# Kernel tuning notes

Measured on AMD Instinct MI355X. Metric: run time of the kernel, lower is better.

The kernel has to match this reference:

```python
import jax, jax.numpy as jnp
import numpy as np

B = 16          # graphs per batch
N = 8192        # nodes per graph (equal-size graphs)
D = 256         # in_channels
RATIO = 0.5
K = int(np.ceil(RATIO * N))   # nodes kept per graph (PyG: ceil(ratio*N))
E = 2_097_152   # total edges (~avg_degree 16)


def setup_inputs() -> dict:
    key = jax.random.key(0)
    k1, k2, k3 = jax.random.split(key, 3)
    x = jax.random.normal(k1, (B * N, D), dtype=jnp.float32)
    # edges confined within each graph: local endpoint ids + graph offset
    local = jax.random.randint(k2, (2, E), 0, N)
    graph_of_edge = jnp.arange(E) // (E // B)            # [E]
    edge_index = local + graph_of_edge[None, :] * N      # [2, E] global node ids
    batch = jnp.repeat(jnp.arange(B), N)                 # [B*N]
    weight = jax.random.normal(k3, (D,), dtype=jnp.float32)  # TopKPooling score weight
    return {"x": x, "edge_index": edge_index, "batch": batch, "weight": weight}


def reference(x, edge_index, batch, weight):
    total = x.shape[0]
    # PyG TopKPooling: score = tanh((x . w) / ||w||)
    score = jnp.tanh((x @ weight) / jnp.linalg.norm(weight))   # [B*N]
    # per-graph top-k (equal-size graphs -> reshape)
    vals, idx = jax.lax.top_k(score.reshape(B, N), K)          # [B, K] each
    perm = (idx + jnp.arange(B)[:, None] * N).reshape(-1)      # [B*K] global kept ids
    x_out = x[perm] * vals.reshape(-1, 1)                      # gate features by score
    batch_out = batch[perm]
    # reindex: kept node i (in perm order) gets new id i, others -1 (PyG filter_adj)
    mapping = jnp.full((total,), -1, dtype=jnp.int32).at[perm].set(
        jnp.arange(B * K, dtype=jnp.int32))
    new_src = mapping[edge_index[0]]
    new_dst = mapping[edge_index[1]]
    kept = (new_src >= 0) & (new_dst >= 0)
    # fixed-shape padded edge_index: surviving edges reindexed, dropped edges = -1
    new_edge_index = jnp.where(kept[None, :], jnp.stack([new_src, new_dst]), -1)
    return x_out, new_edge_index, batch_out
```

## Files before the change

### kernel.cpp

```cpp
#include <hip/hip_runtime.h>

#define BGRAPH  16
#define NPG     8192
#define DIM     256
#define KKEEP   4096
#define TOTALN  (BGRAPH * NPG)
#define TOTKEEP (BGRAPH * KKEEP)
#define NEDGE   2097152
#define NBUCK   8192

using u16 = unsigned short;
using u32 = unsigned int;

__device__ __forceinline__ u32 desc_key(float f) {
  u32 b = __float_as_uint(f);
  u32 s = b ^ ((b & 0x80000000u) ? 0xFFFFFFFFu : 0x80000000u);
  return ~s;
}

__global__ __launch_bounds__(256) void k_score(const float* __restrict__ x,
                                               const float* __restrict__ w,
                                               float* __restrict__ score) {
  int gid  = blockIdx.x * 256 + threadIdx.x;
  int row  = gid >> 6;
  int lane = gid & 63;
  const float4 x4 = *reinterpret_cast<const float4*>(x + (size_t)row * DIM + lane * 4);
  const float4 w4 = *reinterpret_cast<const float4*>(w + lane * 4);
  double dot = (double)x4.x * w4.x + (double)x4.y * w4.y
             + (double)x4.z * w4.z + (double)x4.w * w4.w;
  double w2  = (double)w4.x * w4.x + (double)w4.y * w4.y
             + (double)w4.z * w4.z + (double)w4.w * w4.w;
  #pragma unroll
  for (int off = 32; off > 0; off >>= 1) {
    dot += __shfl_xor(dot, off, 64);
    w2  += __shfl_xor(w2,  off, 64);
  }
  if (lane == 0) score[row] = tanhf((float)(dot / sqrt(w2)));
}

__global__ __launch_bounds__(1024) void k_sort(const float* __restrict__ score,
                                               u32* __restrict__ skey,
                                               u32* __restrict__ bends,
                                               u32* __restrict__ gceil) {
  __shared__ u32 hist[NBUCK];
  __shared__ u32 wsum[16];
  const int g    = blockIdx.x;
  const int tid  = threadIdx.x;
  const int wid  = tid >> 6;
  const int lane = tid & 63;
  const float* gs = score + ((size_t)g << 13);
  u32* skg = skey  + ((size_t)g << 13);
  u32* beg = bends + ((size_t)g << 13);

  #pragma unroll
  for (int i = 0; i < NBUCK / 1024; ++i) hist[tid + i * 1024] = 0;
  __syncthreads();

  u32 kd_[NPG / 1024];
  #pragma unroll
  for (int i = 0; i < NPG / 1024; ++i) {
    kd_[i] = desc_key(gs[tid + i * 1024]);
    atomicAdd(&hist[kd_[i] >> 19], 1u);
  }
  __syncthreads();

  u32 h[8], s = 0;
  #pragma unroll
  for (int j = 0; j < 8; ++j) { h[j] = hist[8 * tid + j]; s += h[j]; }
  u32 inc = s;
  #pragma unroll
  for (int off = 1; off < 64; off <<= 1) {
    u32 t = __shfl_up(inc, off, 64);
    if (lane >= off) inc += t;
  }
  if (lane == 63) wsum[wid] = inc;
  __syncthreads();
  if (tid < 16) {
    u32 v = wsum[tid], vi = v;
    #pragma unroll
    for (int off = 1; off < 16; off <<= 1) {
      u32 t = __shfl_up(vi, off, 64);
      if (tid >= off) vi += t;
    }
    wsum[tid] = vi - v;
  }
  __syncthreads();
  u32 run = inc - s + wsum[wid];
  #pragma unroll
  for (int j = 0; j < 8; ++j) {
    u32 hv  = h[j];
    u32 end = run + hv;
    hist[8 * tid + j] = run;
    beg[8 * tid + j]  = end;
    if (run < KKEEP && end >= KKEEP) gceil[g] = end;
    run = end;
  }
  __syncthreads();

  #pragma unroll
  for (int i = 0; i < NPG / 1024; ++i) {
    int idx = tid + i * 1024;
    u32 kd  = kd_[i];
    u32 pos = atomicAdd(&hist[kd >> 19], 1u);
    skg[pos] = (kd << 13) | (u32)idx;
  }
}

__global__ __launch_bounds__(512) void k_count(const float* __restrict__ score,
                                               const u32* __restrict__ skey,
                                               const u32* __restrict__ bends,
                                               const u32* __restrict__ gceil,
                                               u16* __restrict__ map16) {
  const int g = blockIdx.x >> 4;
  const int p = (blockIdx.x & 15) * 512 + (int)threadIdx.x;
  const size_t gb = ((size_t)g << 13);
  const u32* skg = skey + gb;
  u32 key = skg[p];
  int idx = (int)(key & 0x1FFFu);
  u16* mp = map16 + gb;
  if ((u32)p >= gceil[g]) { mp[idx] = (u16)0xFFFFu; return; }
  u32 b = desc_key(score[gb + idx]) >> 19;
  const u32* beg = bends + gb;
  u32 start = b ? beg[b - 1] : 0;
  u32 end   = beg[b];
  u32 cnt = 0, q = start;
  for (; q + 4 <= end; q += 4) {
    cnt += (skg[q]     < key) + (skg[q + 1] < key)
         + (skg[q + 2] < key) + (skg[q + 3] < key);
  }
  for (; q < end; ++q) cnt += (skg[q] < key);
  u32 rank = start + cnt;
  mp[idx] = (rank < KKEEP) ? (u16)rank : (u16)0xFFFFu;
}

__global__ __launch_bounds__(256) void k_gather(const float* __restrict__ x,
                                                const float* __restrict__ score,
                                                const u16* __restrict__ map16,
                                                float* __restrict__ x_out) {
  int gid  = blockIdx.x * 256 + threadIdx.x;
  int node = gid >> 6;
  int lane = gid & 63;
  u16 rk = map16[node];
  if (rk == 0xFFFFu) return;
  int nid = ((node >> 13) << 12) | (int)rk;
  float val = score[node];
  const float4 v = *reinterpret_cast<const float4*>(x + (size_t)node * DIM + lane * 4);
  float4 o;
  o.x = v.x * val; o.y = v.y * val; o.z = v.z * val; o.w = v.w * val;
  *reinterpret_cast<float4*>(x_out + (size_t)nid * DIM + lane * 4) = o;
}

__global__ __launch_bounds__(256) void k_edges(const int* __restrict__ ei,
                                               const u16* __restrict__ map16,
                                               float* __restrict__ e_out,
                                               float* __restrict__ b_out) {
  int t = blockIdx.x * 256 + threadIdx.x;
  const int4 a = *reinterpret_cast<const int4*>(ei + 4 * (size_t)t);
  const int4 b = *reinterpret_cast<const int4*>(ei + NEDGE + 4 * (size_t)t);
  u16 ra0 = map16[a.x], ra1 = map16[a.y], ra2 = map16[a.z], ra3 = map16[a.w];
  u16 rb0 = map16[b.x], rb1 = map16[b.y], rb2 = map16[b.z], rb3 = map16[b.w];
  float4 eo0, eo1;
  eo0.x = (ra0 != 0xFFFFu && rb0 != 0xFFFFu) ? (float)(((a.x >> 13) << 12) | ra0) : -1.0f;
  eo0.y = (ra1 != 0xFFFFu && rb1 != 0xFFFFu) ? (float)(((a.y >> 13) << 12) | ra1) : -1.0f;
  eo0.z = (ra2 != 0xFFFFu && rb2 != 0xFFFFu) ? (float)(((a.z >> 13) << 12) | ra2) : -1.0f;
  eo0.w = (ra3 != 0xFFFFu && rb3 != 0xFFFFu) ? (float)(((a.w >> 13) << 12) | ra3) : -1.0f;
  eo1.x = (ra0 != 0xFFFFu && rb0 != 0xFFFFu) ? (float)(((b.x >> 13) << 12) | rb0) : -1.0f;
  eo1.y = (ra1 != 0xFFFFu && rb1 != 0xFFFFu) ? (float)(((b.y >> 13) << 12) | rb1) : -1.0f;
  eo1.z = (ra2 != 0xFFFFu && rb2 != 0xFFFFu) ? (float)(((b.z >> 13) << 12) | rb2) : -1.0f;
  eo1.w = (ra3 != 0xFFFFu && rb3 != 0xFFFFu) ? (float)(((b.w >> 13) << 12) | rb3) : -1.0f;
  *reinterpret_cast<float4*>(e_out + 4 * (size_t)t)         = eo0;
  *reinterpret_cast<float4*>(e_out + NEDGE + 4 * (size_t)t) = eo1;
  if (t < TOTKEEP / 4) {
    float4 bo;
    bo.x = (float)((4 * t)     >> 12);
    bo.y = (float)((4 * t + 1) >> 12);
    bo.z = (float)((4 * t + 2) >> 12);
    bo.w = (float)((4 * t + 3) >> 12);
    *reinterpret_cast<float4*>(b_out + 4 * (size_t)t) = bo;
  }
}

extern "C" void kernel_launch(void* const* d_in, const int* in_sizes, int n_in,
                              void* d_out, int out_size, void* d_ws, size_t ws_size,
                              hipStream_t stream) {
  const float* x  = nullptr;
  const int*   ei = nullptr;
  const float* w  = nullptr;
  for (int i = 0; i < n_in; ++i) {
    if      (in_sizes[i] == TOTALN * DIM) x  = (const float*)d_in[i];
    else if (in_sizes[i] == 2 * NEDGE)    ei = (const int*)d_in[i];
    else if (in_sizes[i] == DIM)          w  = (const float*)d_in[i];
  }
  (void)out_size; (void)ws_size;

  float* out   = (float*)d_out;
  float* x_out = out;
  float* e_out = out + (size_t)TOTKEEP * DIM;
  float* b_out = e_out + 2 * (size_t)NEDGE;

  char* ws = (char*)d_ws;
  float* score = (float*)(ws);
  u32*   skey  = (u32*)(ws + (512  << 10));
  u32*   bends = (u32*)(ws + (1024 << 10));
  u16*   map16 = (u16*)(ws + (1536 << 10));
  u32*   gceil = (u32*)(ws + (1792 << 10));

  hipLaunchKernelGGL(k_score,  dim3(TOTALN / 4),  dim3(256),  0, stream, x, w, score);
  hipLaunchKernelGGL(k_sort,   dim3(BGRAPH),      dim3(1024), 0, stream, score, skey, bends, gceil);
  hipLaunchKernelGGL(k_count,  dim3(BGRAPH * 16), dim3(512),  0, stream, score, skey, bends, gceil, map16);
  hipLaunchKernelGGL(k_gather, dim3(TOTALN / 4),  dim3(256),  0, stream, x, score, map16, x_out);
  hipLaunchKernelGGL(k_edges,  dim3(NEDGE / 1024),dim3(256),  0, stream, ei, map16, e_out, b_out);
}
```

Before: 92.84 us.

## Split per-graph bucket sort across eight blocks per graph

```diff
diff --git a/kernel.cpp b/kernel.cpp
--- a/kernel.cpp
+++ b/kernel.cpp
@@ -8,6 +8,7 @@
 #define TOTKEEP (BGRAPH * KKEEP)
 #define NEDGE   2097152
 #define NBUCK   8192
+#define SCHUNK  8
 
 using u16 = unsigned short;
 using u32 = unsigned int;
@@ -43,8 +44,9 @@
                                                u32* __restrict__ bends,
                                                u32* __restrict__ gceil) {
   __shared__ u32 hist[NBUCK];
-  __shared__ u32 wsum[16];
-  const int g    = blockIdx.x;
+  __shared__ u32 acc[NBUCK];
+  const int g    = blockIdx.x >> 3;
+  const int c    = blockIdx.x & (SCHUNK - 1);
   const int tid  = threadIdx.x;
   const int wid  = tid >> 6;
   const int lane = tid & 63;
@@ -53,57 +55,68 @@
   u32* beg = bends + ((size_t)g << 13);
 
   #pragma unroll
-  for (int i = 0; i < NBUCK / 1024; ++i) hist[tid + i * 1024] = 0;
-  __syncthreads();
-
-  u32 kd_[NPG / 1024];
-  #pragma unroll
-  for (int i = 0; i < NPG / 1024; ++i) {
-    kd_[i] = desc_key(gs[tid + i * 1024]);
-    atomicAdd(&hist[kd_[i] >> 19], 1u);
+  for (int i = 0; i < NBUCK / 1024; ++i) {
+    hist[tid + i * 1024] = 0;
+    acc[tid + i * 1024]  = 0;
+  }
+  __syncthreads();
+
+  u32 mykd = 0;
+  #pragma unroll
+  for (int c2 = 0; c2 < SCHUNK; ++c2) {
+    u32 kd = desc_key(gs[c2 * 1024 + tid]);
+    atomicAdd(&hist[kd >> 19], 1u);
+    if (c2 == c) mykd = kd;
+    if (c2 < c)  atomicAdd(&acc[kd >> 19], 1u);
   }
   __syncthreads();
 
   u32 h[8], s = 0;
   #pragma unroll
   for (int j = 0; j < 8; ++j) { h[j] = hist[8 * tid + j]; s += h[j]; }
+  __syncthreads();
   u32 inc = s;
   #pragma unroll
   for (int off = 1; off < 64; off <<= 1) {
     u32 t = __shfl_up(inc, off, 64);
     if (lane >= off) inc += t;
   }
-  if (lane == 63) wsum[wid] = inc;
+  if (lane == 63) hist[wid] = inc;
   __syncthreads();
   if (tid < 16) {
-    u32 v = wsum[tid], vi = v;
+    u32 v = hist[tid], vi = v;
     #pragma unroll
     for (int off = 1; off < 16; off <<= 1) {
       u32 t = __shfl_up(vi, off, 64);
       if (tid >= off) vi += t;
     }
-    wsum[tid] = vi - v;
-  }
-  __syncthreads();
-  u32 run = inc - s + wsum[wid];
+    hist[tid] = vi - v;
+  }
+  __syncthreads();
+  u32 excl = inc - s + hist[wid];
+  __syncthreads();
+  u32 run = excl;
   #pragma unroll
   for (int j = 0; j < 8; ++j) {
-    u32 hv  = h[j];
-    u32 end = run + hv;
+    u32 end = run + h[j];
     hist[8 * tid + j] = run;
-    beg[8 * tid + j]  = end;
-    if (run < KKEEP && end >= KKEEP) gceil[g] = end;
+    if (c == 0) {
+      beg[8 * tid + j] = end;
+      if (run < KKEEP && end >= KKEEP) gceil[g] = end;
+    }
     run = end;
   }
   __syncthreads();
 
   #pragma unroll
-  for (int i = 0; i < NPG / 1024; ++i) {
-    int idx = tid + i * 1024;
-    u32 kd  = kd_[i];
-    u32 pos = atomicAdd(&hist[kd >> 19], 1u);
-    skg[pos] = (kd << 13) | (u32)idx;
-  }
+  for (int i = 0; i < NBUCK / 1024; ++i) {
+    int b = tid + i * 1024;
+    acc[b] += hist[b];
+  }
+  __syncthreads();
+
+  u32 pos = atomicAdd(&acc[mykd >> 19], 1u);
+  skg[pos] = (mykd << 13) | (u32)(c * 1024 + tid);
 }
 
 __global__ __launch_bounds__(512) void k_count(const float* __restrict__ score,
@@ -205,9 +218,9 @@
   u16*   map16 = (u16*)(ws + (1536 << 10));
   u32*   gceil = (u32*)(ws + (1792 << 10));
 
-  hipLaunchKernelGGL(k_score,  dim3(TOTALN / 4),  dim3(256),  0, stream, x, w, score);
-  hipLaunchKernelGGL(k_sort,   dim3(BGRAPH),      dim3(1024), 0, stream, score, skey, bends, gceil);
-  hipLaunchKernelGGL(k_count,  dim3(BGRAPH * 16), dim3(512),  0, stream, score, skey, bends, gceil, map16);
-  hipLaunchKernelGGL(k_gather, dim3(TOTALN / 4),  dim3(256),  0, stream, x, score, map16, x_out);
-  hipLaunchKernelGGL(k_edges,  dim3(NEDGE / 1024),dim3(256),  0, stream, ei, map16, e_out, b_out);
-}
+  hipLaunchKernelGGL(k_score,  dim3(TOTALN / 4),        dim3(256),  0, stream, x, w, score);
+  hipLaunchKernelGGL(k_sort,   dim3(BGRAPH * SCHUNK),   dim3(1024), 0, stream, score, skey, bends, gceil);
+  hipLaunchKernelGGL(k_count,  dim3(BGRAPH * 16),       dim3(512),  0, stream, score, skey, bends, gceil, map16);
+  hipLaunchKernelGGL(k_gather, dim3(TOTALN / 4),        dim3(256),  0, stream, x, score, map16, x_out);
+  hipLaunchKernelGGL(k_edges,  dim3(NEDGE / 1024),      dim3(256),  0, stream, ei, map16, e_out, b_out);
+}
```

Measured after the change: 91.12 us. Within noise of the previous version (-1.9%).

## Fuse all phases into one cooperative persistent kernel with grid syncs

Applied to the files above, without the earlier changes.

```diff
diff --git a/kernel.cpp b/kernel.cpp
--- a/kernel.cpp
+++ b/kernel.cpp
@@ -1,4 +1,7 @@
 #include <hip/hip_runtime.h>
+#include <hip/hip_cooperative_groups.h>
+
+namespace cg = cooperative_groups;
 
 #define BGRAPH  16
 #define NPG     8192
@@ -9,6 +12,9 @@
 #define NEDGE   2097152
 #define NBUCK   8192
 
+#define NBLK    256
+#define NTHR    1024
+
 using u16 = unsigned short;
 using u32 = unsigned int;
 
@@ -18,34 +24,37 @@
   return ~s;
 }
 
-__global__ __launch_bounds__(256) void k_score(const float* __restrict__ x,
-                                               const float* __restrict__ w,
-                                               float* __restrict__ score) {
-  int gid  = blockIdx.x * 256 + threadIdx.x;
-  int row  = gid >> 6;
-  int lane = gid & 63;
-  const float4 x4 = *reinterpret_cast<const float4*>(x + (size_t)row * DIM + lane * 4);
+__device__ __forceinline__ void phase_score(int gwave, int lane,
+                                            const float* __restrict__ x,
+                                            const float* __restrict__ w,
+                                            float* __restrict__ score) {
   const float4 w4 = *reinterpret_cast<const float4*>(w + lane * 4);
-  double dot = (double)x4.x * w4.x + (double)x4.y * w4.y
-             + (double)x4.z * w4.z + (double)x4.w * w4.w;
-  double w2  = (double)w4.x * w4.x + (double)w4.y * w4.y
-             + (double)w4.z * w4.z + (double)w4.w * w4.w;
-  #pragma unroll
-  for (int off = 32; off > 0; off >>= 1) {
-    dot += __shfl_xor(dot, off, 64);
-    w2  += __shfl_xor(w2,  off, 64);
-  }
-  if (lane == 0) score[row] = tanhf((float)(dot / sqrt(w2)));
-}
-
-__global__ __launch_bounds__(1024) void k_sort(const float* __restrict__ score,
-                                               u32* __restrict__ skey,
-                                               u32* __restrict__ bends,
-                                               u32* __restrict__ gceil) {
+  double w2 = (double)w4.x * w4.x + (double)w4.y * w4.y
+            + (double)w4.z * w4.z + (double)w4.w * w4.w;
+  #pragma unroll
+  for (int off = 32; off > 0; off >>= 1) w2 += __shfl_xor(w2, off, 64);
+  const double rn = sqrt(w2);
+  #pragma unroll 4
+  for (int i = 0; i < 32; ++i) {
+    int row = gwave * 32 + i;
+    const float4 x4 = *reinterpret_cast<const float4*>(x + (size_t)row * DIM + lane * 4);
+    double dot = (double)x4.x * w4.x + (double)x4.y * w4.y
+               + (double)x4.z * w4.z + (double)x4.w * w4.w;
+    #pragma unroll
+    for (int off = 32; off > 0; off >>= 1) dot += __shfl_xor(dot, off, 64);
+    if (lane == 0) score[row] = tanhf((float)(dot / rn));
+  }
+}
+
+__device__ __forceinline__ void phase_sort(int blk, int tid,
+                                           const float* __restrict__ score,
+                                           u32* __restrict__ skey,
+                                           u32* __restrict__ bends,
+                                           u32* __restrict__ gceil) {
   __shared__ u32 hist[NBUCK];
   __shared__ u32 wsum[16];
-  const int g    = blockIdx.x;
-  const int tid  = threadIdx.x;
+  if (blk >= BGRAPH) return;
+  const int g    = blk;
   const int wid  = tid >> 6;
   const int lane = tid & 63;
   const float* gs = score + ((size_t)g << 13);
@@ -53,13 +62,13 @@
   u32* beg = bends + ((size_t)g << 13);
 
   #pragma unroll
-  for (int i = 0; i < NBUCK / 1024; ++i) hist[tid + i * 1024] = 0;
-  __syncthreads();
-
-  u32 kd_[NPG / 1024];
-  #pragma unroll
-  for (int i = 0; i < NPG / 1024; ++i) {
-    kd_[i] = desc_key(gs[tid + i * 1024]);
+  for (int i = 0; i < NBUCK / NTHR; ++i) hist[tid + i * NTHR] = 0;
+  __syncthreads();
+
+  u32 kd_[NPG / NTHR];
+  #pragma unroll
+  for (int i = 0; i < NPG / NTHR; ++i) {
+    kd_[i] = desc_key(gs[tid + i * NTHR]);
     atomicAdd(&hist[kd_[i] >> 19], 1u);
   }
   __syncthreads();
@@ -98,27 +107,28 @@
   __syncthreads();
 
   #pragma unroll
-  for (int i = 0; i < NPG / 1024; ++i) {
-    int idx = tid + i * 1024;
-    u32 kd  = kd_[i];
-    u32 pos = atomicAdd(&hist[kd >> 19], 1u);
-    skg[pos] = (kd << 13) | (u32)idx;
-  }
-}
-
-__global__ __launch_bounds__(512) void k_count(const float* __restrict__ score,
-                                               const u32* __restrict__ skey,
-                                               const u32* __restrict__ bends,
-                                               const u32* __restrict__ gceil,
-                                               u16* __restrict__ map16) {
-  const int g = blockIdx.x >> 4;
-  const int p = (blockIdx.x & 15) * 512 + (int)threadIdx.x;
+  for (int i = 0; i < NPG / NTHR; ++i) {
+    int idx = tid + i * NTHR;
+    u32 pos = atomicAdd(&hist[kd_[i] >> 19], 1u);
+    skg[pos] = (kd_[i] << 13) | (u32)idx;
+  }
+}
+
+__device__ __forceinline__ void phase_count(int t,
+                                            const float* __restrict__ score,
+                                            const u32* __restrict__ skey,
+                                            const u32* __restrict__ bends,
+                                            const u32* __restrict__ gceil,
+                                            u16* __restrict__ map16,
+                                            u16* __restrict__ inv) {
+  if (t >= TOTALN) return;
+  const int g = t >> 13;
+  const int p = t & (NPG - 1);
   const size_t gb = ((size_t)g << 13);
   const u32* skg = skey + gb;
   u32 key = skg[p];
   int idx = (int)(key & 0x1FFFu);
-  u16* mp = map16 + gb;
-  if ((u32)p >= gceil[g]) { mp[idx] = (u16)0xFFFFu; return; }
+  if ((u32)p >= gceil[g]) { map16[gb + idx] = (u16)0xFFFFu; return; }
   u32 b = desc_key(score[gb + idx]) >> 19;
   const u32* beg = bends + gb;
   u32 start = b ? beg[b - 1] : 0;
@@ -130,54 +140,118 @@
   }
   for (; q < end; ++q) cnt += (skg[q] < key);
   u32 rank = start + cnt;
-  mp[idx] = (rank < KKEEP) ? (u16)rank : (u16)0xFFFFu;
-}
-
-__global__ __launch_bounds__(256) void k_gather(const float* __restrict__ x,
-                                                const float* __restrict__ score,
-                                                const u16* __restrict__ map16,
-                                                float* __restrict__ x_out) {
-  int gid  = blockIdx.x * 256 + threadIdx.x;
-  int node = gid >> 6;
-  int lane = gid & 63;
-  u16 rk = map16[node];
-  if (rk == 0xFFFFu) return;
-  int nid = ((node >> 13) << 12) | (int)rk;
-  float val = score[node];
-  const float4 v = *reinterpret_cast<const float4*>(x + (size_t)node * DIM + lane * 4);
-  float4 o;
-  o.x = v.x * val; o.y = v.y * val; o.z = v.z * val; o.w = v.w * val;
-  *reinterpret_cast<float4*>(x_out + (size_t)nid * DIM + lane * 4) = o;
-}
-
-__global__ __launch_bounds__(256) void k_edges(const int* __restrict__ ei,
-                                               const u16* __restrict__ map16,
+  if (rank < KKEEP) {
+    map16[gb + idx] = (u16)rank;
+    inv[((u32)g << 12) | rank] = (u16)idx;
+  } else {
+    map16[gb + idx] = (u16)0xFFFFu;
+  }
+}
+
+__device__ __forceinline__ void phase_gather(int gwave, int lane,
+                                             const float* __restrict__ x,
+                                             const float* __restrict__ score,
+                                             const u16* __restrict__ inv,
+                                             float* __restrict__ x_out) {
+  #pragma unroll 4
+  for (int i = 0; i < 16; ++i) {
+    int r = gwave * 16 + i;
+    int idx  = (int)inv[r];
+    int node = ((r >> 12) << 13) | idx;
+    float val = score[node];
+    const float4 v = *reinterpret_cast<const float4*>(x + (size_t)node * DIM + lane * 4);
+    float4 o;
+    o.x = v.x * val; o.y = v.y * val; o.z = v.z * val; o.w = v.w * val;
+    *reinterpret_cast<float4*>(x_out + (size_t)r * DIM + lane * 4) = o;
+  }
+}
+
+__device__ __forceinline__ void edges4(const int4 a, const int4 b,
+                                       const u16* __restrict__ map16,
+                                       float4& es, float4& ed) {
+  u16 ra0 = map16[a.x], ra1 = map16[a.y], ra2 = map16[a.z], ra3 = map16[a.w];
+  u16 rb0 = map16[b.x], rb1 = map16[b.y], rb2 = map16[b.z], rb3 = map16[b.w];
+  bool k0 = (ra0 != 0xFFFFu) && (rb0 != 0xFFFFu);
+  bool k1 = (ra1 != 0xFFFFu) && (rb1 != 0xFFFFu);
+  bool k2 = (ra2 != 0xFFFFu) && (rb2 != 0xFFFFu);
+  bool k3 = (ra3 != 0xFFFFu) && (rb3 != 0xFFFFu);
+  es.x = k0 ? (float)(((a.x >> 13) << 12) | ra0) : -1.0f;
+  es.y = k1 ? (float)(((a.y >> 13) << 12) | ra1) : -1.0f;
+  es.z = k2 ? (float)(((a.z >> 13) << 12) | ra2) : -1.0f;
+  es.w = k3 ? (float)(((a.w >> 13) << 12) | ra3) : -1.0f;
+  ed.x = k0 ? (float)(((b.x >> 13) << 12) | rb0) : -1.0f;
+  ed.y = k1 ? (float)(((b.y >> 13) << 12) | rb1) : -1.0f;
+  ed.z = k2 ? (float)(((b.z >> 13) << 12) | rb2) : -1.0f;
+  ed.w = k3 ? (float)(((b.w >> 13) << 12) | rb3) : -1.0f;
+}
+
+__device__ __forceinline__ void phase_edges(int t,
+                                            const int* __restrict__ ei,
+                                            const u16* __restrict__ map16,
+                                            float* __restrict__ e_out,
+                                            float* __restrict__ b_out) {
+  size_t e8 = (size_t)t * 8;
+  const int4 a0 = *reinterpret_cast<const int4*>(ei + e8);
+  const int4 a1 = *reinterpret_cast<const int4*>(ei + e8 + 4);
+  const int4 d0 = *reinterpret_cast<const int4*>(ei + NEDGE + e8);
+  const int4 d1 = *reinterpret_cast<const int4*>(ei + NEDGE + e8 + 4);
+  float4 s0, dd0, s1, dd1;
+  edges4(a0, d0, map16, s0, dd0);
+  edges4(a1, d1, map16, s1, dd1);
+  *reinterpret_cast<float4*>(e_out + e8)             = s0;
+  *reinterpret_cast<float4*>(e_out + e8 + 4)         = s1;
+  *reinterpret_cast<float4*>(e_out + NEDGE + e8)     = dd0;
+  *reinterpret_cast<float4*>(e_out + NEDGE + e8 + 4) = dd1;
+  if (t < TOTKEEP / 4) {
+    float gf = (float)(t >> 10);
+    float4 bo; bo.x = gf; bo.y = gf; bo.z = gf; bo.w = gf;
+    *reinterpret_cast<float4*>(b_out + 4 * (size_t)t) = bo;
+  }
+}
+
+__global__ __launch_bounds__(NTHR) void k_mega(const float* __restrict__ x,
+                                               const float* __restrict__ w,
+                                               const int* __restrict__ ei,
+                                               float* __restrict__ score,
+                                               u32* __restrict__ skey,
+                                               u32* __restrict__ bends,
+                                               u32* __restrict__ gceil,
+                                               u16* __restrict__ map16,
+                                               u16* __restrict__ inv,
+                                               float* __restrict__ x_out,
                                                float* __restrict__ e_out,
                                                float* __restrict__ b_out) {
-  int t = blockIdx.x * 256 + threadIdx.x;
-  const int4 a = *reinterpret_cast<const int4*>(ei + 4 * (size_t)t);
-  const int4 b = *reinterpret_cast<const int4*>(ei + NEDGE + 4 * (size_t)t);
-  u16 ra0 = map16[a.x], ra1 = map16[a.y], ra2 = map16[a.z], ra3 = map16[a.w];
-  u16 rb0 = map16[b.x], rb1 = map16[b.y], rb2 = map16[b.z], rb3 = map16[b.w];
-  float4 eo0, eo1;
-  eo0.x = (ra0 != 0xFFFFu && rb0 != 0xFFFFu) ? (float)(((a.x >> 13) << 12) | ra0) : -1.0f;
-  eo0.y = (ra1 != 0xFFFFu && rb1 != 0xFFFFu) ? (float)(((a.y >> 13) << 12) | ra1) : -1.0f;
-  eo0.z = (ra2 != 0xFFFFu && rb2 != 0xFFFFu) ? (float)(((a.z >> 13) << 12) | ra2) : -1.0f;
-  eo0.w = (ra3 != 0xFFFFu && rb3 != 0xFFFFu) ? (float)(((a.w >> 13) << 12) | ra3) : -1.0f;
-  eo1.x = (ra0 != 0xFFFFu && rb0 != 0xFFFFu) ? (float)(((b.x >> 13) << 12) | rb0) : -1.0f;
-  eo1.y = (ra1 != 0xFFFFu && rb1 != 0xFFFFu) ? (float)(((b.y >> 13) << 12) | rb1) : -1.0f;
-  eo1.z = (ra2 != 0xFFFFu && rb2 != 0xFFFFu) ? (float)(((b.z >> 13) << 12) | rb2) : -1.0f;
-  eo1.w = (ra3 != 0xFFFFu && rb3 != 0xFFFFu) ? (float)(((b.w >> 13) << 12) | rb3) : -1.0f;
-  *reinterpret_cast<float4*>(e_out + 4 * (size_t)t)         = eo0;
-  *reinterpret_cast<float4*>(e_out + NEDGE + 4 * (size_t)t) = eo1;
-  if (t < TOTKEEP / 4) {
-    float4 bo;
-    bo.x = (float)((4 * t)     >> 12);
-    bo.y = (float)((4 * t + 1) >> 12);
-    bo.z = (float)((4 * t + 2) >> 12);
-    bo.w = (float)((4 * t + 3) >> 12);
-    *reinterpret_cast<float4*>(b_out + 4 * (size_t)t) = bo;
-  }
+  cg::grid_group grid = cg::this_grid();
+  const int blk = blockIdx.x, tid = threadIdx.x;
+  const int lane  = tid & 63;
+  const int gwave = blk * (NTHR / 64) + (tid >> 6);
+  const int t     = blk * NTHR + tid;
+
+  phase_score(gwave, lane, x, w, score);
+  grid.sync();
+  phase_sort(blk, tid, score, skey, bends, gceil);
+  grid.sync();
+  phase_count(t, score, skey, bends, gceil, map16, inv);
+  grid.sync();
+  phase_gather(gwave, lane, x, score, inv, x_out);
+  phase_edges(t, ei, map16, e_out, b_out);
+}
+
+__global__ __launch_bounds__(NTHR) void k_pA(const float* x, const float* w, float* score) {
+  phase_score(blockIdx.x * (NTHR / 64) + (threadIdx.x >> 6), threadIdx.x & 63, x, w, score);
+}
+__global__ __launch_bounds__(NTHR) void k_pB(const float* score, u32* skey, u32* bends, u32* gceil) {
+  phase_sort(blockIdx.x, threadIdx.x, score, skey, bends, gceil);
+}
+__global__ __launch_bounds__(NTHR) void k_pC(const float* score, const u32* skey, const u32* bends,
+                                             const u32* gceil, u16* map16, u16* inv) {
+  phase_count(blockIdx.x * NTHR + threadIdx.x, score, skey, bends, gceil, map16, inv);
+}
+__global__ __launch_bounds__(NTHR) void k_pDE(const float* x, const float* score, const u16* inv,
+                                              const int* ei, const u16* map16,
+                                              float* x_out, float* e_out, float* b_out) {
+  phase_gather(blockIdx.x * (NTHR / 64) + (threadIdx.x >> 6), threadIdx.x & 63, x, score, inv, x_out);
+  phase_edges(blockIdx.x * NTHR + threadIdx.x, ei, map16, e_out, b_out);
 }
 
 extern "C" void kernel_launch(void* const* d_in, const int* in_sizes, int n_in,
@@ -203,11 +277,18 @@
   u32*   skey  = (u32*)(ws + (512  << 10));
   u32*   bends = (u32*)(ws + (1024 << 10));
   u16*   map16 = (u16*)(ws + (1536 << 10));
-  u32*   gceil = (u32*)(ws + (1792 << 10));
-
-  hipLaunchKernelGGL(k_score,  dim3(TOTALN / 4),  dim3(256),  0, stream, x, w, score);
-  hipLaunchKernelGGL(k_sort,   dim3(BGRAPH),      dim3(1024), 0, stream, score, skey, bends, gceil);
-  hipLaunchKernelGGL(k_count,  dim3(BGRAPH * 16), dim3(512),  0, stream, score, skey, bends, gceil, map16);
-  hipLaunchKernelGGL(k_gather, dim3(TOTALN / 4),  dim3(256),  0, stream, x, score, map16, x_out);
-  hipLaunchKernelGGL(k_edges,  dim3(NEDGE / 1024),dim3(256),  0, stream, ei, map16, e_out, b_out);
-}
+  u16*   inv   = (u16*)(ws + (1792 << 10));
+  u32*   gceil = (u32*)(ws + (1920 << 10));
+
+  void* args[] = {(void*)&x, (void*)&w, (void*)&ei, (void*)&score, (void*)&skey,
+                  (void*)&bends, (void*)&gceil, (void*)&map16, (void*)&inv,
+                  (void*)&x_out, (void*)&e_out, (void*)&b_out};
+  hipError_t err = hipLaunchCooperativeKernel((const void*)k_mega, dim3(NBLK), dim3(NTHR),
+                                              args, 0, stream);
+  if (err != hipSuccess) {
+    hipLaunchKernelGGL(k_pA,  dim3(NBLK), dim3(NTHR), 0, stream, x, w, score);
+    hipLaunchKernelGGL(k_pB,  dim3(NBLK), dim3(NTHR), 0, stream, score, skey, bends, gceil);
+    hipLaunchKernelGGL(k_pC,  dim3(NBLK), dim3(NTHR), 0, stream, score, skey, bends, gceil, map16, inv);
+    hipLaunchKernelGGL(k_pDE, dim3(NBLK), dim3(NTHR), 0, stream, x, score, inv, ei, map16, x_out, e_out, b_out);
+  }
+}
```

New measurement: 180.7 us. +94.6%, slower.

## Fuse gather and edge kernels, gather via inverse map, prune sort scatter

Applied to the files above, without the earlier changes.

```diff
diff --git a/kernel.cpp b/kernel.cpp
--- a/kernel.cpp
+++ b/kernel.cpp
@@ -20,8 +20,10 @@
 
 __global__ __launch_bounds__(256) void k_score(const float* __restrict__ x,
                                                const float* __restrict__ w,
-                                               float* __restrict__ score) {
+                                               float* __restrict__ score,
+                                               u32* __restrict__ map32) {
   int gid  = blockIdx.x * 256 + threadIdx.x;
+  if (gid < TOTALN / 2) map32[gid] = 0xFFFFFFFFu;
   int row  = gid >> 6;
   int lane = gid & 63;
   const float4 x4 = *reinterpret_cast<const float4*>(x + (size_t)row * DIM + lane * 4);
@@ -44,6 +46,7 @@
                                                u32* __restrict__ gceil) {
   __shared__ u32 hist[NBUCK];
   __shared__ u32 wsum[16];
+  __shared__ u32 sbb;
   const int g    = blockIdx.x;
   const int tid  = threadIdx.x;
   const int wid  = tid >> 6;
@@ -92,17 +95,23 @@
     u32 end = run + hv;
     hist[8 * tid + j] = run;
     beg[8 * tid + j]  = end;
-    if (run < KKEEP && end >= KKEEP) gceil[g] = end;
+    if (run < KKEEP && end >= KKEEP) {
+      gceil[g] = end;
+      sbb = (u32)(8 * tid + j);
+    }
     run = end;
   }
   __syncthreads();
 
+  const u32 bb = sbb;
   #pragma unroll
   for (int i = 0; i < NPG / 1024; ++i) {
-    int idx = tid + i * 1024;
-    u32 kd  = kd_[i];
-    u32 pos = atomicAdd(&hist[kd >> 19], 1u);
-    skg[pos] = (kd << 13) | (u32)idx;
+    u32 kd = kd_[i];
+    u32 b  = kd >> 19;
+    if (b <= bb) {
+      u32 pos = atomicAdd(&hist[b], 1u);
+      skg[pos] = (kd << 13) | (u32)(tid + i * 1024);
+    }
   }
 }
 
@@ -110,15 +119,15 @@
                                                const u32* __restrict__ skey,
                                                const u32* __restrict__ bends,
                                                const u32* __restrict__ gceil,
-                                               u16* __restrict__ map16) {
+                                               u16* __restrict__ map16,
+                                               u16* __restrict__ inv) {
   const int g = blockIdx.x >> 4;
   const int p = (blockIdx.x & 15) * 512 + (int)threadIdx.x;
+  if ((u32)p >= gceil[g]) return;
   const size_t gb = ((size_t)g << 13);
   const u32* skg = skey + gb;
   u32 key = skg[p];
   int idx = (int)(key & 0x1FFFu);
-  u16* mp = map16 + gb;
-  if ((u32)p >= gceil[g]) { mp[idx] = (u16)0xFFFFu; return; }
   u32 b = desc_key(score[gb + idx]) >> 19;
   const u32* beg = bends + gb;
   u32 start = b ? beg[b - 1] : 0;
@@ -130,52 +139,83 @@
   }
   for (; q < end; ++q) cnt += (skg[q] < key);
   u32 rank = start + cnt;
-  mp[idx] = (rank < KKEEP) ? (u16)rank : (u16)0xFFFFu;
-}
-
-__global__ __launch_bounds__(256) void k_gather(const float* __restrict__ x,
-                                                const float* __restrict__ score,
-                                                const u16* __restrict__ map16,
-                                                float* __restrict__ x_out) {
-  int gid  = blockIdx.x * 256 + threadIdx.x;
-  int node = gid >> 6;
-  int lane = gid & 63;
-  u16 rk = map16[node];
-  if (rk == 0xFFFFu) return;
-  int nid = ((node >> 13) << 12) | (int)rk;
-  float val = score[node];
-  const float4 v = *reinterpret_cast<const float4*>(x + (size_t)node * DIM + lane * 4);
-  float4 o;
-  o.x = v.x * val; o.y = v.y * val; o.z = v.z * val; o.w = v.w * val;
-  *reinterpret_cast<float4*>(x_out + (size_t)nid * DIM + lane * 4) = o;
-}
-
-__global__ __launch_bounds__(256) void k_edges(const int* __restrict__ ei,
-                                               const u16* __restrict__ map16,
-                                               float* __restrict__ e_out,
-                                               float* __restrict__ b_out) {
-  int t = blockIdx.x * 256 + threadIdx.x;
-  const int4 a = *reinterpret_cast<const int4*>(ei + 4 * (size_t)t);
-  const int4 b = *reinterpret_cast<const int4*>(ei + NEDGE + 4 * (size_t)t);
-  u16 ra0 = map16[a.x], ra1 = map16[a.y], ra2 = map16[a.z], ra3 = map16[a.w];
-  u16 rb0 = map16[b.x], rb1 = map16[b.y], rb2 = map16[b.z], rb3 = map16[b.w];
-  float4 eo0, eo1;
-  eo0.x = (ra0 != 0xFFFFu && rb0 != 0xFFFFu) ? (float)(((a.x >> 13) << 12) | ra0) : -1.0f;
-  eo0.y = (ra1 != 0xFFFFu && rb1 != 0xFFFFu) ? (float)(((a.y >> 13) << 12) | ra1) : -1.0f;
-  eo0.z = (ra2 != 0xFFFFu && rb2 != 0xFFFFu) ? (float)(((a.z >> 13) << 12) | ra2) : -1.0f;
-  eo0.w = (ra3 != 0xFFFFu && rb3 != 0xFFFFu) ? (float)(((a.w >> 13) << 12) | ra3) : -1.0f;
-  eo1.x = (ra0 != 0xFFFFu && rb0 != 0xFFFFu) ? (float)(((b.x >> 13) << 12) | rb0) : -1.0f;
-  eo1.y = (ra1 != 0xFFFFu && rb1 != 0xFFFFu) ? (float)(((b.y >> 13) << 12) | rb1) : -1.0f;
-  eo1.z = (ra2 != 0xFFFFu && rb2 != 0xFFFFu) ? (float)(((b.z >> 13) << 12) | rb2) : -1.0f;
-  eo1.w = (ra3 != 0xFFFFu && rb3 != 0xFFFFu) ? (float)(((b.w >> 13) << 12) | rb3) : -1.0f;
-  *reinterpret_cast<float4*>(e_out + 4 * (size_t)t)         = eo0;
-  *reinterpret_cast<float4*>(e_out + NEDGE + 4 * (size_t)t) = eo1;
+  if (rank < KKEEP) {
+    map16[gb + idx] = (u16)rank;
+    inv[((u32)g << 12) | rank] = (u16)idx;
+  }
+}
+
+#define GB 16384
+#define EB 1024
+
+__global__ __launch_bounds__(256) void k_ge(const float* __restrict__ x,
+                                            const float* __restrict__ score,
+                                            const u16* __restrict__ inv,
+                                            const int* __restrict__ ei,
+                                            const u16* __restrict__ map16,
+                                            float* __restrict__ x_out,
+                                            float* __restrict__ e_out,
+                                            float* __restrict__ b_out) {
+  const int blk = blockIdx.x;
+  const int tid = threadIdx.x;
+  if (blk < GB) {
+    int r    = blk * 4 + (tid >> 6);
+    int lane = tid & 63;
+    int idx  = (int)inv[r];
+    int node = ((r >> 12) << 13) | idx;
+    float val = score[node];
+    const float4 v = *reinterpret_cast<const float4*>(x + (size_t)node * DIM + lane * 4);
+    float4 o;
+    o.x = v.x * val; o.y = v.y * val; o.z = v.z * val; o.w = v.w * val;
+    *reinterpret_cast<float4*>(x_out + (size_t)r * DIM + lane * 4) = o;
+    return;
+  }
+  int t = (blk - GB) * 256 + tid;
+  size_t e8 = (size_t)t * 8;
+  const int4 a0 = *reinterpret_cast<const int4*>(ei + e8);
+  const int4 a1 = *reinterpret_cast<const int4*>(ei + e8 + 4);
+  const int4 d0 = *reinterpret_cast<const int4*>(ei + NEDGE + e8);
+  const int4 d1 = *reinterpret_cast<const int4*>(ei + NEDGE + e8 + 4);
+  float4 s0, s1, dd0, dd1;
+  {
+    u16 ra0 = map16[a0.x], ra1 = map16[a0.y], ra2 = map16[a0.z], ra3 = map16[a0.w];
+    u16 rb0 = map16[d0.x], rb1 = map16[d0.y], rb2 = map16[d0.z], rb3 = map16[d0.w];
+    bool k0 = (ra0 != 0xFFFFu) && (rb0 != 0xFFFFu);
+    bool k1 = (ra1 != 0xFFFFu) && (rb1 != 0xFFFFu);
+    bool k2 = (ra2 != 0xFFFFu) && (rb2 != 0xFFFFu);
+    bool k3 = (ra3 != 0xFFFFu) && (rb3 != 0xFFFFu);
+    s0.x  = k0 ? (float)(((a0.x >> 13) << 12) | ra0) : -1.0f;
+    s0.y  = k1 ? (float)(((a0.y >> 13) << 12) | ra1) : -1.0f;
+    s0.z  = k2 ? (float)(((a0.z >> 13) << 12) | ra2) : -1.0f;
+    s0.w  = k3 ? (float)(((a0.w >> 13) << 12) | ra3) : -1.0f;
+    dd0.x = k0 ? (float)(((d0.x >> 13) << 12) | rb0) : -1.0f;
+    dd0.y = k1 ? (float)(((d0.y >> 13) << 12) | rb1) : -1.0f;
+    dd0.z = k2 ? (float)(((d0.z >> 13) << 12) | rb2) : -1.0f;
+    dd0.w = k3 ? (float)(((d0.w >> 13) << 12) | rb3) : -1.0f;
+  }
+  {
+    u16 ra0 = map16[a1.x], ra1 = map16[a1.y], ra2 = map16[a1.z], ra3 = map16[a1.w];
+    u16 rb0 = map16[d1.x], rb1 = map16[d1.y], rb2 = map16[d1.z], rb3 = map16[d1.w];
+    bool k0 = (ra0 != 0xFFFFu) && (rb0 != 0xFFFFu);
+    bool k1 = (ra1 != 0xFFFFu) && (rb1 != 0xFFFFu);
+    bool k2 = (ra2 != 0xFFFFu) && (rb2 != 0xFFFFu);
+    bool k3 = (ra3 != 0xFFFFu) && (rb3 != 0xFFFFu);
+    s1.x  = k0 ? (float)(((a1.x >> 13) << 12) | ra0) : -1.0f;
+    s1.y  = k1 ? (float)(((a1.y >> 13) << 12) | ra1) : -1.0f;
+    s1.z  = k2 ? (float)(((a1.z >> 13) << 12) | ra2) : -1.0f;
+    s1.w  = k3 ? (float)(((a1.w >> 13) << 12) | ra3) : -1.0f;
+    dd1.x = k0 ? (float)(((d1.x >> 13) << 12) | rb0) : -1.0f;
+    dd1.y = k1 ? (float)(((d1.y >> 13) << 12) | rb1) : -1.0f;
+    dd1.z = k2 ? (float)(((d1.z >> 13) << 12) | rb2) : -1.0f;
+    dd1.w = k3 ? (float)(((d1.w >> 13) << 12) | rb3) : -1.0f;
+  }
+  *reinterpret_cast<float4*>(e_out + e8)             = s0;
+  *reinterpret_cast<float4*>(e_out + e8 + 4)         = s1;
+  *reinterpret_cast<float4*>(e_out + NEDGE + e8)     = dd0;
+  *reinterpret_cast<float4*>(e_out + NEDGE + e8 + 4) = dd1;
   if (t < TOTKEEP / 4) {
-    float4 bo;
-    bo.x = (float)((4 * t)     >> 12);
-    bo.y = (float)((4 * t + 1) >> 12);
-    bo.z = (float)((4 * t + 2) >> 12);
-    bo.w = (float)((4 * t + 3) >> 12);
+    float gf = (float)(t >> 10);
+    float4 bo; bo.x = gf; bo.y = gf; bo.z = gf; bo.w = gf;
     *reinterpret_cast<float4*>(b_out + 4 * (size_t)t) = bo;
   }
 }
@@ -203,11 +243,15 @@
   u32*   skey  = (u32*)(ws + (512  << 10));
   u32*   bends = (u32*)(ws + (1024 << 10));
   u16*   map16 = (u16*)(ws + (1536 << 10));
-  u32*   gceil = (u32*)(ws + (1792 << 10));
-
-  hipLaunchKernelGGL(k_score,  dim3(TOTALN / 4),  dim3(256),  0, stream, x, w, score);
-  hipLaunchKernelGGL(k_sort,   dim3(BGRAPH),      dim3(1024), 0, stream, score, skey, bends, gceil);
-  hipLaunchKernelGGL(k_count,  dim3(BGRAPH * 16), dim3(512),  0, stream, score, skey, bends, gceil, map16);
-  hipLaunchKernelGGL(k_gather, dim3(TOTALN / 4),  dim3(256),  0, stream, x, score, map16, x_out);
-  hipLaunchKernelGGL(k_edges,  dim3(NEDGE / 1024),dim3(256),  0, stream, ei, map16, e_out, b_out);
-}
+  u16*   inv   = (u16*)(ws + (1792 << 10));
+  u32*   gceil = (u32*)(ws + (1920 << 10));
+
+  hipLaunchKernelGGL(k_score, dim3(TOTALN / 4),  dim3(256),  0, stream,
+                     x, w, score, (u32*)map16);
+  hipLaunchKernelGGL(k_sort,  dim3(BGRAPH),      dim3(1024), 0, stream,
+                     score, skey, bends, gceil);
+  hipLaunchKernelGGL(k_count, dim3(BGRAPH * 16), dim3(512),  0, stream,
+                     score, skey, bends, gceil, map16, inv);
+  hipLaunchKernelGGL(k_ge,    dim3(GB + EB),     dim3(256),  0, stream,
+                     x, score, inv, ei, map16, x_out, e_out, b_out);
+}
```

Measured after the change: 92.23 us. Within noise of the previous version (-0.7%).
